# Kernel optimization log

Measured on AMD Instinct MI355X. Metric: run time of the kernel, lower is better.

The kernel has to match this reference:

```python
import jax, jax.numpy as jnp
import numpy as np

H = 8      # n_heads
HD = 64    # per-head channels (out_channels in __init__, before *= n_heads)


def setup_inputs() -> dict:
    key = jax.random.key(0)
    ks = jax.random.split(key, 10)
    B, C, N = 4, 256, 2048
    O = H * HD
    s = 1.0 / np.sqrt(C).astype(np.float32)
    return {
        "x": jax.random.normal(ks[0], (B, C, N), dtype=jnp.float32),
        "y": jax.random.normal(ks[1], (B, C, N), dtype=jnp.float32),
        "Wq": jax.random.normal(ks[2], (O, C), dtype=jnp.float32) * s,
        "bq": jnp.zeros((O,), dtype=jnp.float32),
        "Wk": jax.random.normal(ks[3], (O, C), dtype=jnp.float32) * s,
        "bk": jnp.zeros((O,), dtype=jnp.float32),
        "Wv": jax.random.normal(ks[4], (O, C), dtype=jnp.float32) * s,
        "bv": jnp.zeros((O,), dtype=jnp.float32),
        "Wp": jax.random.normal(ks[5], (HD, C), dtype=jnp.float32) * s,  # residual projection, bias=False
        "gamma": jax.random.uniform(ks[6], (H, 1, 1, 1), dtype=jnp.float32) + 0.001,
    }


def _conv1x1(W, b, t):
    # 1x1 Conv1d: (O,C) x (B,C,N) -> (B,O,N)
    out = jnp.einsum('oc,bcn->bon', W, t)
    return out if b is None else out + b[None, :, None]


def _heads(t):
    # (B, H*HD, N) -> (H, B, N, HD); channel split into contiguous per-head chunks
    B, _, N = t.shape
    return t.reshape(B, H, HD, N).transpose(1, 0, 3, 2)


def reference(x, y, Wq, bq, Wk, bk, Wv, bv, Wp, gamma):
    # q/k/v projections via 1x1 convs (kernel_size=1, 'stride_effective' padding => same length)
    q = _heads(_conv1x1(Wq, bq, x))   # (H,B,N,HD)
    k = _heads(_conv1x1(Wk, bk, y))   # (H,B,N,HD)
    v = _heads(_conv1x1(Wv, bv, y))   # (H,B,N,HD)

    # energy = bmm(Q, K^T); softmax over last dim (no mask)
    energy = jnp.einsum('hbnd,hbmd->hbnm', q, k)          # (H,B,N,N)
    attn = jax.nn.softmax(energy, axis=-1)

    # out = bmm(attention.transpose(-2,-1), V)  (note the transpose in the original)
    out = jnp.einsum('hbnm,hbnd->hbmd', attn, v)          # (H,B,N,HD)

    # gamma-weighted residual blend with projected y
    yp = _conv1x1(Wp, None, y).transpose(0, 2, 1)         # (B,N,HD)
    g = gamma.reshape(H, 1, 1, 1)
    out = (g * out + yp[None]) / (1.0 + g)                # (H,B,N,HD)
    return out
```

## Files before the change

### kernel.cpp

```cpp
#include <hip/hip_runtime.h>
#include <math.h>

#define B_DIM 4
#define C_DIM 256
#define N_DIM 2048
#define H_DIM 8
#define HD    64
#define HB    32
#define NTOK  (B_DIM * N_DIM)
#define LOG2E 1.44269504f

typedef __attribute__((ext_vector_type(8))) short bf16x8;
typedef __attribute__((ext_vector_type(4))) float f32x4;

static __device__ __forceinline__ short f2bf(float f) {
    unsigned u = __builtin_bit_cast(unsigned, f);
    u += 0x7fffu + ((u >> 16) & 1u);
    return (short)(u >> 16);
}
static __device__ __forceinline__ float bf2f(short s) {
    unsigned u = ((unsigned)(unsigned short)s) << 16;
    return __builtin_bit_cast(float, u);
}
static __device__ __forceinline__ float fx2(float x) {
#if __has_builtin(__builtin_amdgcn_exp2f)
    return __builtin_amdgcn_exp2f(x);
#else
    return exp2f(x);
#endif
}
static __device__ __forceinline__ unsigned pk_bf16(float a, float b) {
#if __has_builtin(__builtin_amdgcn_cvt_pk_bf16_f32)
    auto v = __builtin_amdgcn_cvt_pk_bf16_f32(a, b);
    return __builtin_bit_cast(unsigned, v);
#else
    unsigned ua = __builtin_bit_cast(unsigned, a);
    unsigned ub = __builtin_bit_cast(unsigned, b);
    return ((ua + 0x8000u) >> 16) | ((ub + 0x8000u) & 0xffff0000u);
#endif
}

#define MFMA16(A, Bv, Cv) __builtin_amdgcn_mfma_f32_16x16x32_bf16(A, Bv, Cv, 0, 0, 0)


__global__ __launch_bounds__(256) void cast_all(
    const float* __restrict__ X, const float* __restrict__ Y,
    const float* __restrict__ Wq, const float* __restrict__ Wk,
    const float* __restrict__ Wv, const float* __restrict__ Wp,
    short* __restrict__ XS, short* __restrict__ YS,
    short* __restrict__ WSx, short* __restrict__ WSy)
{
    const int z = blockIdx.z;
    const int t = threadIdx.x;

    if (z == 8) {
        int base = (blockIdx.y * 32 + blockIdx.x) * 256 + t;
#pragma unroll
        for (int rep = 0; rep < 2; ++rep) {
            int gid = base + rep * 32768;
            if (gid >= 51200) break;
            int lane = gid & 63, chunk = gid >> 6;
            int lo = lane & 15, quad = lane >> 4;
            const float* src; short* dst;
            if (chunk < 256) {
                int ot = chunk >> 3, ks = chunk & 7;
                src = Wq + (size_t)(ot * 16 + lo) * C_DIM + ks * 32 + quad * 8;
                dst = WSx + (size_t)chunk * 512 + lane * 8;
            } else {
                int ch = chunk - 256;
                int ot = ch >> 3, ks = ch & 7;
                int row = ot * 16 + lo;
                const float* basep = (row < 512) ? (Wk + (size_t)row * C_DIM)
                                   : (row < 1024) ? (Wv + (size_t)(row - 512) * C_DIM)
                                                  : (Wp + (size_t)(row - 1024) * C_DIM);
                src = basep + ks * 32 + quad * 8;
                dst = WSy + (size_t)ch * 512 + lane * 8;
            }
            bf16x8 o;
#pragma unroll
            for (int j = 0; j < 8; ++j) o[j] = f2bf(src[j]);
            *(bf16x8*)dst = o;
        }
        return;
    }

    const float* src = (z < 4) ? X : Y;
    short* dst = (z < 4) ? XS : YS;
    const int b = z & 3, c0 = blockIdx.y * 64, n0 = blockIdx.x * 64;
    __shared__ float L[64][65];
    for (int i = t; i < 4096; i += 256) {
        int cc = i >> 6, nn = i & 63;
        L[cc][nn] = src[((size_t)b * C_DIM + c0 + cc) * N_DIM + n0 + nn];
    }
    __syncthreads();
#pragma unroll
    for (int half = 0; half < 2; ++half) {
        int cid = half * 256 + t;
        int lane = cid & 63, fi = cid >> 6;
        int ksl = fi & 1, rtl = fi >> 1;
        int lo = lane & 15, quad = lane >> 4;
        bf16x8 o;
#pragma unroll
        for (int j = 0; j < 8; ++j) o[j] = f2bf(L[ksl * 32 + quad * 8 + j][rtl * 16 + lo]);
        int rt = b * 128 + (n0 >> 4) + rtl;
        int ks = (c0 >> 5) + ksl;
        *(bf16x8*)(dst + ((size_t)(rt * 8 + ks) * 64 + lane) * 8) = o;
    }
}

__global__ __launch_bounds__(256) void proj_all(
    const short* __restrict__ WSx, const short* __restrict__ WSy,
    const short* __restrict__ XS, const short* __restrict__ YS,
    const float* __restrict__ bq, const float* __restrict__ bk,
    const float* __restrict__ bv,
    short* __restrict__ QS, short* __restrict__ KS,
    short* __restrict__ VSu, float* __restrict__ Yo)
{
    const int oy = blockIdx.y;
    const bool isq = oy < 8;
    const short* WS = isq ? WSx : WSy;
    const short* Xs = isq ? XS : YS;
    const int oyl = isq ? oy : oy - 8;
    const int o0 = oyl * 64;
    const int tok0 = blockIdx.x * 128;
    const int t = threadIdx.x, wave = t >> 6, lane = t & 63;
    const int lo = lane & 15, quad = lane >> 4;

    __shared__ __align__(16) char smem[34816];

    const int ot = oyl * 4 + wave;
    const int rt0 = tok0 >> 4;
    const f32x4 czero = {0.f, 0.f, 0.f, 0.f};

    f32x4 acc[8];
#pragma unroll
    for (int i = 0; i < 8; ++i) acc[i] = czero;

#pragma unroll 2
    for (int ks = 0; ks < 8; ++ks) {
        bf16x8 a = *(const bf16x8*)(WS + ((size_t)(ot * 8 + ks) * 64 + lane) * 8);
#pragma unroll
        for (int nt = 0; nt < 8; ++nt) {
            bf16x8 bx = *(const bf16x8*)(Xs + ((size_t)((rt0 + nt) * 8 + ks) * 64 + lane) * 8);
            acc[nt] = MFMA16(a, bx, acc[nt]);
        }
    }

    const int b = tok0 >> 11;
    const int n0b = tok0 & (N_DIM - 1);

    if (oy < 16) {
        short* T = (short*)smem;
        const float* bias = isq ? bq : bk;
        const float scale = isq ? LOG2E : 1.f;
        float bvr[4];
#pragma unroll
        for (int r = 0; r < 4; ++r) bvr[r] = bias[o0 + wave * 16 + quad * 4 + r];
#pragma unroll
        for (int nt = 0; nt < 8; ++nt) {
            short4 pk;
            pk.x = f2bf((acc[nt][0] + bvr[0]) * scale);
            pk.y = f2bf((acc[nt][1] + bvr[1]) * scale);
            pk.z = f2bf((acc[nt][2] + bvr[2]) * scale);
            pk.w = f2bf((acc[nt][3] + bvr[3]) * scale);
            *(short4*)(T + (nt * 16 + lo) * 72 + wave * 16 + quad * 4) = pk;
        }
        __syncthreads();
        const int h = oyl;
        const int hb = h * 4 + b;
        short* dst = isq ? QS : KS;
#pragma unroll
        for (int s = 0; s < 4; ++s) {
            int cid = s * 256 + t;
            int ln = cid & 63, fi = cid >> 6;
            int ksd = fi & 1, rtl = fi >> 1;
            bf16x8 v = *(const bf16x8*)(T + (rtl * 16 + (ln & 15)) * 72 + ksd * 32 + (ln >> 4) * 8);
            *(bf16x8*)(dst + (((size_t)(hb * 128 + (n0b >> 4) + rtl) * 2 + ksd) * 512 + ln * 8)) = v;
        }
    } else if (oy < 24) {
        short* T2 = (short*)smem;
        float bvr[4];
#pragma unroll
        for (int r = 0; r < 4; ++r) bvr[r] = bv[o0 - 512 + wave * 16 + quad * 4 + r];
#pragma unroll
        for (int nt = 0; nt < 8; ++nt)
#pragma unroll
            for (int r = 0; r < 4; ++r) {
                int ol = wave * 16 + quad * 4 + r;
                T2[ol * 136 + nt * 16 + lo] = f2bf(acc[nt][r] + bvr[r]);
            }
        __syncthreads();
        const int h = oy - 16;
        const int hb = h * 4 + b;
#pragma unroll
        for (int s = 0; s < 4; ++s) {
            int cid = s * 256 + t;
            int ln = cid & 63, fi = cid >> 6;
            int dt = fi & 3, ksd = (fi >> 2) & 1, nbl = fi >> 3;
            int dl = dt * 16 + (ln & 15);
            int tkl = nbl * 64 + ksd * 32 + (ln >> 4) * 8;
            bf16x8 v = *(const bf16x8*)(T2 + dl * 136 + tkl);
            int nbg = (n0b >> 6) + nbl;
            *(bf16x8*)(VSu + ((size_t)(((hb * 32 + nbg) * 2 + ksd) * 4 + dt) * 64 + ln) * 8) = v;
        }
    } else {
        float* T3 = (float*)smem;
#pragma unroll
        for (int nt = 0; nt < 8; ++nt) {
            float4 f;
            f.x = acc[nt][0]; f.y = acc[nt][1]; f.z = acc[nt][2]; f.w = acc[nt][3];
            *(float4*)(T3 + (nt * 16 + lo) * 68 + wave * 16 + quad * 4) = f;
        }
        __syncthreads();
#pragma unroll
        for (int s = 0; s < 8; ++s) {
            int cid = s * 256 + t;
            int row = cid >> 4, c4 = (cid & 15) * 4;
            float4 f = *(const float4*)(T3 + row * 68 + c4);
            *(float4*)(Yo + ((size_t)(tok0 + row)) * 64 + c4) = f;
        }
    }
}

__global__ __launch_bounds__(256, 4) void rowsum_mfma(
    const short* __restrict__ QS, const short* __restrict__ KS,
    float* __restrict__ RSp, float* __restrict__ RSpW)
{
    const int id = blockIdx.x;
    const int hb = ((id & 7) << 2) | ((id >> 3) & 3);
    const int zq = (id >> 5) & 3;
    const int n0 = (id >> 7) * 256;
    const int t = threadIdx.x, wave = t >> 6, lane = t & 63;
    const int lo = lane & 15, quad = lane >> 4;
    const f32x4 czero = {0.f, 0.f, 0.f, 0.f};

    bf16x8 a0[4], a1[4];
#pragma unroll
    for (int s = 0; s < 4; ++s) {
        int rt = (n0 >> 4) + s * 4 + wave;
        a0[s] = *(const bf16x8*)(QS + ((size_t)(hb * 128 + rt) * 2 + 0) * 512 + lane * 8);
        a1[s] = *(const bf16x8*)(QS + ((size_t)(hb * 128 + rt) * 2 + 1) * 512 + lane * 8);
    }

    float sm[4][4];
#pragma unroll
    for (int s = 0; s < 4; ++s)
#pragma unroll
        for (int r = 0; r < 4; ++r) sm[s][r] = 0.f;

    const short* kp = KS + ((size_t)(hb * 128) * 2) * 512 + lane * 8
                    + (size_t)zq * (N_DIM / 4 / 16) * 2 * 512;
    for (int m0 = 0; m0 < N_DIM / 4; m0 += 64) {
#pragma unroll
        for (int mt = 0; mt < 4; ++mt) {
            bf16x8 b0 = *(const bf16x8*)(kp + (mt * 2 + 0) * 512);
            bf16x8 b1 = *(const bf16x8*)(kp + (mt * 2 + 1) * 512);
#pragma unroll
            for (int s = 0; s < 4; ++s) {
                f32x4 c = MFMA16(a0[s], b0, czero);
                c = MFMA16(a1[s], b1, c);
#pragma unroll
                for (int r = 0; r < 4; ++r) sm[s][r] += fx2(c[r]);
            }
        }
        kp += 8 * 512;
    }

#pragma unroll
    for (int sft = 1; sft < 16; sft <<= 1)
#pragma unroll
        for (int s = 0; s < 4; ++s)
#pragma unroll
            for (int r = 0; r < 4; ++r) sm[s][r] += __shfl_xor(sm[s][r], sft);

    if (lo == 0) {
        float* dst = (zq < 2) ? (RSp  + (size_t)zq * HB * N_DIM)
                              : (RSpW + (size_t)(zq - 2) * HB * N_DIM);
#pragma unroll
        for (int s = 0; s < 4; ++s) {
            int row = n0 + s * 64 + wave * 16 + quad * 4;
#pragma unroll
            for (int r = 0; r < 4; ++r)
                dst[(size_t)hb * N_DIM + row + r] = sm[s][r];
        }
    }
}

__global__ __launch_bounds__(256) void v_scale(
    const short* __restrict__ VSu, const float* __restrict__ RSp,
    const float* __restrict__ RSpW, short* __restrict__ VS)
{
    int t = blockIdx.x * 256 + threadIdx.x;
    int lane = t & 63, fidx = t >> 6;
    int ks = (fidx >> 2) & 1, nb = (fidx >> 3) & 31, hb = fidx >> 8;
    int n = nb * 64 + ks * 32 + (lane >> 4) * 8;
    bf16x8 v = *(const bf16x8*)(VSu + (size_t)t * 8);
    const float* r0 = RSp  + (size_t)hb * N_DIM + n;
    const float* r1 = r0 + (size_t)HB * N_DIM;
    const float* r2 = RSpW + (size_t)hb * N_DIM + n;
    const float* r3 = r2 + (size_t)HB * N_DIM;
    bf16x8 o;
#pragma unroll
    for (int j = 0; j < 8; ++j)
        o[j] = f2bf(bf2f(v[j]) / ((r0[j] + r1[j]) + (r2[j] + r3[j])));
    *(bf16x8*)(VS + (size_t)t * 8) = o;
}

__global__ __launch_bounds__(256, 2) void attnout_mfma(
    const short* __restrict__ QS, const short* __restrict__ KS,
    const short* __restrict__ VS,
    short* __restrict__ PA0, short* __restrict__ PA1)
{
    const int id = blockIdx.x;
    const int hb = ((id & 7) << 2) | ((id >> 3) & 3);
    const int z = (id >> 5) & 1;
    const int m0 = (id >> 6) * 256;

    __shared__ __align__(16) char smem[32768];
    short* Pl = (short*)smem;

    const int t = threadIdx.x, wave = t >> 6, lane = t & 63;
    const int lo = lane & 15, quad = lane >> 4;
    const f32x4 czero = {0.f, 0.f, 0.f, 0.f};

    bf16x8 bk0[4], bk1[4];
#pragma unroll
    for (int s = 0; s < 4; ++s) {
        int rt = (m0 >> 4) + s * 4 + wave;
        bk0[s] = *(const bf16x8*)(KS + ((size_t)(hb * 128 + rt) * 2 + 0) * 512 + lane * 8);
        bk1[s] = *(const bf16x8*)(KS + ((size_t)(hb * 128 + rt) * 2 + 1) * 512 + lane * 8);
    }

    f32x4 oacc[4][4];
#pragma unroll
    for (int s = 0; s < 4; ++s)
#pragma unroll
        for (int dt = 0; dt < 4; ++dt) oacc[s][dt] = czero;

    const short* qp = QS + ((size_t)(hb * 128) * 2) * 512 + lane * 8
                    + (size_t)z * (N_DIM / 2 / 16) * 2 * 512;
    const short* vp = VS + ((size_t)(hb * 32) * 8) * 512 + lane * 8
                    + (size_t)z * (N_DIM / 2 / 64) * 8 * 512;
    short* prow = Pl + (wave * 16 + lo) * 64;
    const int lh = lo & 7;
    const int NIT = N_DIM / 2 / 64;

    f32x4 c[4][4];

    {
#pragma unroll
        for (int nt = 0; nt < 4; ++nt) {
            bf16x8 a0 = *(const bf16x8*)(qp + (nt * 2 + 0) * 512);
            bf16x8 a1 = *(const bf16x8*)(qp + (nt * 2 + 1) * 512);
#pragma unroll
            for (int s = 0; s < 4; ++s) {
                c[nt][s] = MFMA16(a0, bk0[s], czero);
                c[nt][s] = MFMA16(a1, bk1[s], c[nt][s]);
            }
        }
        qp += 8 * 512;
    }

    for (int i = 0; i < NIT - 1; ++i) {
        bf16x8 a0[4], a1[4];
#pragma unroll
        for (int nt = 0; nt < 4; ++nt) {
            a0[nt] = *(const bf16x8*)(qp + (nt * 2 + 0) * 512);
            a1[nt] = *(const bf16x8*)(qp + (nt * 2 + 1) * 512);
        }
#pragma unroll
        for (int nt = 0; nt < 4; ++nt)
#pragma unroll
            for (int s = 0; s < 4; ++s) {
                uint2 pk;
                pk.x = pk_bf16(fx2(c[nt][s][0]), fx2(c[nt][s][1]));
                pk.y = pk_bf16(fx2(c[nt][s][2]), fx2(c[nt][s][3]));
                int chunk = nt * 2 + (quad >> 1);
                *(uint2*)(prow + s * 4096 + (((chunk ^ lh) << 3) | ((quad & 1) << 2))) = pk;
            }
        __builtin_amdgcn_s_setprio(1);
#pragma unroll
        for (int nt = 0; nt < 4; ++nt)
#pragma unroll
            for (int s = 0; s < 4; ++s) {
                c[nt][s] = MFMA16(a0[nt], bk0[s], czero);
                c[nt][s] = MFMA16(a1[nt], bk1[s], c[nt][s]);
            }
        __builtin_amdgcn_s_setprio(0);
#pragma unroll
        for (int ks = 0; ks < 2; ++ks) {
            bf16x8 ap[4];
#pragma unroll
            for (int s = 0; s < 4; ++s)
                ap[s] = *(const bf16x8*)(prow + s * 4096 + (((ks * 4 + quad) ^ lh) << 3));
#pragma unroll
            for (int dt = 0; dt < 4; ++dt) {
                bf16x8 bv = *(const bf16x8*)(vp + (ks * 4 + dt) * 512);
#pragma unroll
                for (int s = 0; s < 4; ++s)
                    oacc[s][dt] = MFMA16(ap[s], bv, oacc[s][dt]);
            }
        }
        qp += 8 * 512;
        vp += 8 * 512;
    }

#pragma unroll
    for (int nt = 0; nt < 4; ++nt)
#pragma unroll
        for (int s = 0; s < 4; ++s) {
            uint2 pk;
            pk.x = pk_bf16(fx2(c[nt][s][0]), fx2(c[nt][s][1]));
            pk.y = pk_bf16(fx2(c[nt][s][2]), fx2(c[nt][s][3]));
            int chunk = nt * 2 + (quad >> 1);
            *(uint2*)(prow + s * 4096 + (((chunk ^ lh) << 3) | ((quad & 1) << 2))) = pk;
        }
#pragma unroll
    for (int ks = 0; ks < 2; ++ks) {
        bf16x8 ap[4];
#pragma unroll
        for (int s = 0; s < 4; ++s)
            ap[s] = *(const bf16x8*)(prow + s * 4096 + (((ks * 4 + quad) ^ lh) << 3));
#pragma unroll
        for (int dt = 0; dt < 4; ++dt) {
            bf16x8 bv = *(const bf16x8*)(vp + (ks * 4 + dt) * 512);
#pragma unroll
            for (int s = 0; s < 4; ++s)
                oacc[s][dt] = MFMA16(ap[s], bv, oacc[s][dt]);
        }
    }

    short* PA = z ? PA1 : PA0;
    float* T = (float*)smem;
#pragma unroll
    for (int s = 0; s < 4; ++s) {
        __syncthreads();
#pragma unroll
        for (int dt = 0; dt < 4; ++dt)
#pragma unroll
            for (int r = 0; r < 4; ++r)
                T[(wave * 16 + quad * 4 + r) * 68 + dt * 16 + lo] = oacc[s][dt][r];
        __syncthreads();
#pragma unroll
        for (int it = 0; it < 2; ++it) {
            int idx = it * 256 + t;
            int rowl = idx >> 3, dg = (idx & 7) * 8;
            float4 f0 = *(const float4*)(T + rowl * 68 + dg);
            float4 f1 = *(const float4*)(T + rowl * 68 + dg + 4);
            uint4 o;
            o.x = pk_bf16(f0.x, f0.y);
            o.y = pk_bf16(f0.z, f0.w);
            o.z = pk_bf16(f1.x, f1.y);
            o.w = pk_bf16(f1.z, f1.w);
            int m = m0 + s * 64 + rowl;
            *(uint4*)(PA + ((size_t)(hb * N_DIM + m)) * 64 + dg) = o;
        }
    }
}

__global__ __launch_bounds__(256) void combine_out(
    const short* __restrict__ PA0, const short* __restrict__ PA1,
    const float* __restrict__ YP, const float* __restrict__ gamma,
    float* __restrict__ out)
{
    size_t flat = ((size_t)blockIdx.x * 256 + threadIdx.x) * 8;
    int d  = (int)(flat & 63);
    int n  = (int)((flat >> 6) & (N_DIM - 1));
    int hb = (int)(flat >> 17);
    int h = hb >> 2, b = hb & 3;
    float g = gamma[h];
    float inv = 1.f / (1.f + g);
    float gi = g * inv;
    bf16x8 p0 = *(const bf16x8*)(PA0 + flat);
    bf16x8 p1 = *(const bf16x8*)(PA1 + flat);
    const float* yp = YP + ((size_t)b * N_DIM + n) * HD + d;
    float o[8];
#pragma unroll
    for (int j = 0; j < 8; ++j)
        o[j] = gi * (bf2f(p0[j]) + bf2f(p1[j])) + inv * yp[j];
    float4 o0 = {o[0], o[1], o[2], o[3]};
    float4 o1 = {o[4], o[5], o[6], o[7]};
    *(float4*)(out + flat) = o0;
    *(float4*)(out + flat + 4) = o1;
}

extern "C" void kernel_launch(void* const* d_in, const int* in_sizes, int n_in,
                              void* d_out, int out_size, void* d_ws, size_t ws_size,
                              hipStream_t stream) {
    const float* x     = (const float*)d_in[0];
    const float* y     = (const float*)d_in[1];
    const float* Wq    = (const float*)d_in[2];
    const float* bq    = (const float*)d_in[3];
    const float* Wk    = (const float*)d_in[4];
    const float* bk    = (const float*)d_in[5];
    const float* Wv    = (const float*)d_in[6];
    const float* bv    = (const float*)d_in[7];
    const float* Wp    = (const float*)d_in[8];
    const float* gamma = (const float*)d_in[9];
    float* out = (float*)d_out;

    const size_t XEL  = (size_t)B_DIM * C_DIM * N_DIM;
    const size_t QKV  = (size_t)HB * N_DIM * HD;

    short* XS  = (short*)d_ws;
    short* YS  = XS + XEL;
    short* WSx = YS + XEL;
    short* WSy = WSx + 512 * C_DIM;
    short* QS  = WSy + 1088 * C_DIM;
    short* KS  = QS + QKV;
    short* VSu = KS + QKV;
    short* VS  = VSu + QKV;
    float* YPb = (float*)(VS + QKV);
    float* RSp = YPb + (size_t)B_DIM * N_DIM * HD;
    short* PA0 = XS;
    short* PA1 = VSu;
    float* RSpW = (float*)WSx;

    dim3 blk(256);
    cast_all<<<dim3(N_DIM / 64, C_DIM / 64, 9), blk, 0, stream>>>(
        x, y, Wq, Wk, Wv, Wp, XS, YS, WSx, WSy);

    proj_all<<<dim3(NTOK / 128, 25), blk, 0, stream>>>(
        WSx, WSy, XS, YS, bq, bk, bv, QS, KS, VSu, YPb);

    rowsum_mfma<<<dim3(1024), blk, 0, stream>>>(QS, KS, RSp, RSpW);
    v_scale<<<dim3(2048), blk, 0, stream>>>(VSu, RSp, RSpW, VS);
    attnout_mfma<<<dim3(512), blk, 0, stream>>>(QS, KS, VS, PA0, PA1);
    combine_out<<<dim3(2048), blk, 0, stream>>>(PA0, PA1, YPb, gamma, out);
}
```

Before: 189.5 us.

## Stage V tiles through double-buffered LDS via async global_load_lds

New measurement: 184.8 us. -2.5%, faster.

```diff
diff --git a/kernel.cpp b/kernel.cpp
--- a/kernel.cpp
+++ b/kernel.cpp
@@ -1,5 +1,6 @@
 #include <hip/hip_runtime.h>
 #include <math.h>
+#include <stdint.h>
 
 #define B_DIM 4
 #define C_DIM 256
@@ -37,6 +38,16 @@
     unsigned ua = __builtin_bit_cast(unsigned, a);
     unsigned ub = __builtin_bit_cast(unsigned, b);
     return ((ua + 0x8000u) >> 16) | ((ub + 0x8000u) & 0xffff0000u);
+#endif
+}
+
+static __device__ __forceinline__ void gll16(const void* g, void* ldsbase, int lane) {
+#if __has_builtin(__builtin_amdgcn_global_load_lds)
+    __builtin_amdgcn_global_load_lds(
+        (const __attribute__((address_space(1))) void*)(uintptr_t)(g),
+        (__attribute__((address_space(3))) void*)(uintptr_t)(ldsbase), 16, 0, 0);
+#else
+    *(bf16x8*)((char*)ldsbase + lane * 16) = *(const bf16x8*)g;
 #endif
 }
 
@@ -316,8 +327,9 @@
     const int z = (id >> 5) & 1;
     const int m0 = (id >> 6) * 256;
 
-    __shared__ __align__(16) char smem[32768];
+    __shared__ __align__(16) char smem[49152];
     short* Pl = (short*)smem;
+    char* Vst = smem + 32768;
 
     const int t = threadIdx.x, wave = t >> 6, lane = t & 63;
     const int lo = lane & 15, quad = lane >> 4;
@@ -339,8 +351,8 @@
 
     const short* qp = QS + ((size_t)(hb * 128) * 2) * 512 + lane * 8
                     + (size_t)z * (N_DIM / 2 / 16) * 2 * 512;
-    const short* vp = VS + ((size_t)(hb * 32) * 8) * 512 + lane * 8
-                    + (size_t)z * (N_DIM / 2 / 64) * 8 * 512;
+    const short* vp0 = VS + ((size_t)(hb * 32) * 8) * 512 + lane * 8
+                     + (size_t)z * (N_DIM / 2 / 64) * 8 * 512;
     short* prow = Pl + (wave * 16 + lo) * 64;
     const int lh = lo & 7;
     const int NIT = N_DIM / 2 / 64;
@@ -348,6 +360,12 @@
     f32x4 c[4][4];
 
     {
+        const short* src = vp0;
+        gll16(src + (size_t)wave * 512,       Vst + wave * 1024, lane);
+        gll16(src + (size_t)(wave + 4) * 512, Vst + (wave + 4) * 1024, lane);
+    }
+
+    {
 #pragma unroll
         for (int nt = 0; nt < 4; ++nt) {
             bf16x8 a0 = *(const bf16x8*)(qp + (nt * 2 + 0) * 512);
@@ -360,8 +378,15 @@
         }
         qp += 8 * 512;
     }
+    __syncthreads();
 
     for (int i = 0; i < NIT - 1; ++i) {
+        {
+            const short* src = vp0 + ((size_t)(i + 1) * 8) * 512;
+            char* dst = Vst + ((i + 1) & 1) * 8192;
+            gll16(src + (size_t)wave * 512,       dst + wave * 1024, lane);
+            gll16(src + (size_t)(wave + 4) * 512, dst + (wave + 4) * 1024, lane);
+        }
         bf16x8 a0[4], a1[4];
 #pragma unroll
         for (int nt = 0; nt < 4; ++nt) {
@@ -387,22 +412,25 @@
                 c[nt][s] = MFMA16(a1[nt], bk1[s], c[nt][s]);
             }
         __builtin_amdgcn_s_setprio(0);
-#pragma unroll
-        for (int ks = 0; ks < 2; ++ks) {
-            bf16x8 ap[4];
-#pragma unroll
-            for (int s = 0; s < 4; ++s)
-                ap[s] = *(const bf16x8*)(prow + s * 4096 + (((ks * 4 + quad) ^ lh) << 3));
-#pragma unroll
-            for (int dt = 0; dt < 4; ++dt) {
-                bf16x8 bv = *(const bf16x8*)(vp + (ks * 4 + dt) * 512);
+        {
+            const char* vb = Vst + (i & 1) * 8192;
+#pragma unroll
+            for (int ks = 0; ks < 2; ++ks) {
+                bf16x8 ap[4];
 #pragma unroll
                 for (int s = 0; s < 4; ++s)
-                    oacc[s][dt] = MFMA16(ap[s], bv, oacc[s][dt]);
+                    ap[s] = *(const bf16x8*)(prow + s * 4096 + (((ks * 4 + quad) ^ lh) << 3));
+#pragma unroll
+                for (int dt = 0; dt < 4; ++dt) {
+                    bf16x8 bv = *(const bf16x8*)(vb + (ks * 4 + dt) * 1024 + lane * 16);
+#pragma unroll
+                    for (int s = 0; s < 4; ++s)
+                        oacc[s][dt] = MFMA16(ap[s], bv, oacc[s][dt]);
+                }
             }
         }
         qp += 8 * 512;
-        vp += 8 * 512;
+        __syncthreads();
     }
 
 #pragma unroll
@@ -415,18 +443,21 @@
             int chunk = nt * 2 + (quad >> 1);
             *(uint2*)(prow + s * 4096 + (((chunk ^ lh) << 3) | ((quad & 1) << 2))) = pk;
         }
-#pragma unroll
-    for (int ks = 0; ks < 2; ++ks) {
-        bf16x8 ap[4];
-#pragma unroll
-        for (int s = 0; s < 4; ++s)
-            ap[s] = *(const bf16x8*)(prow + s * 4096 + (((ks * 4 + quad) ^ lh) << 3));
-#pragma unroll
-        for (int dt = 0; dt < 4; ++dt) {
-            bf16x8 bv = *(const bf16x8*)(vp + (ks * 4 + dt) * 512);
+    {
+        const char* vb = Vst + ((NIT - 1) & 1) * 8192;
+#pragma unroll
+        for (int ks = 0; ks < 2; ++ks) {
+            bf16x8 ap[4];
 #pragma unroll
             for (int s = 0; s < 4; ++s)
-                oacc[s][dt] = MFMA16(ap[s], bv, oacc[s][dt]);
+                ap[s] = *(const bf16x8*)(prow + s * 4096 + (((ks * 4 + quad) ^ lh) << 3));
+#pragma unroll
+            for (int dt = 0; dt < 4; ++dt) {
+                bf16x8 bv = *(const bf16x8*)(vb + (ks * 4 + dt) * 1024 + lane * 16);
+#pragma unroll
+                for (int s = 0; s < 4; ++s)
+                    oacc[s][dt] = MFMA16(ap[s], bv, oacc[s][dt]);
+            }
         }
     }
 
```
